# Performance work log

Measured on AMD Instinct MI355X. Metric: run time of the kernel, lower is better.

Reference implementation:

```python
import jax, jax.numpy as jnp
import numpy as np

N = 50000      # nodes
E = 800000     # edges (before self loops)
D_IN = 256
D_H = 256
D_OUT = 64     # num_classes
SLOPE = 0.01   # leaky_relu slope


def setup_inputs() -> dict:
    key = jax.random.key(0)
    ks = jax.random.split(key, 8)
    x = jax.random.normal(ks[0], (N, D_IN), dtype=jnp.float32)
    edge_index = jax.random.randint(ks[1], (2, E), 0, N, dtype=jnp.int32)
    s = 0.05
    W1 = jax.random.normal(ks[2], (D_H, D_IN), dtype=jnp.float32) * s
    b1 = jnp.zeros((D_H,), dtype=jnp.float32)
    W2 = jax.random.normal(ks[3], (D_H, D_H), dtype=jnp.float32) * s
    b2 = jnp.zeros((D_H,), dtype=jnp.float32)
    W3 = jax.random.normal(ks[4], (D_OUT, D_H), dtype=jnp.float32) * s
    b3 = jnp.zeros((D_OUT,), dtype=jnp.float32)
    return {"x": x, "edge_index": edge_index, "W1": W1, "b1": b1,
            "W2": W2, "b2": b2, "W3": W3, "b3": b3}


def _gcn_layer(x, W, b, src, dst):
    # PyG GCNConv: h = x @ W^T; out[dst] += d^{-1/2}[src] d^{-1/2}[dst] * h[src]; out += b
    h = x @ W.T                                             # [N, out]
    ones = jnp.ones(src.shape[0], dtype=h.dtype)
    deg = jax.ops.segment_sum(ones, dst, num_segments=N)    # includes self loops
    dinv = jnp.where(deg > 0, jax.lax.rsqrt(deg), 0.0)
    norm = dinv[src] * dinv[dst]                            # [E+N]
    msg = h[src] * norm[:, None]                            # gather + scale
    out = jax.ops.segment_sum(msg, dst, num_segments=N)     # scatter-add
    return out + b


def reference(x, edge_index, W1, b1, W2, b2, W3, b3):
    src, dst = edge_index[0], edge_index[1]
    loop = jnp.arange(N, dtype=src.dtype)                   # add self loops
    src = jnp.concatenate([src, loop])
    dst = jnp.concatenate([dst, loop])
    act = lambda h: jax.nn.leaky_relu(h, negative_slope=SLOPE)
    h1 = act(_gcn_layer(x, W1, b1, src, dst))
    h2 = act(_gcn_layer(h1, W2, b2, src, dst))
    logits = _gcn_layer(h2, W3, b3, src, dst)               # no activation on last layer
    return (h1, h2, logits)
```

## Files before the change

kernel.cpp:

```cpp
#include <hip/hip_runtime.h>

#define N_NODES 50000
#define E_EDGES 800000
#define SLOPE 0.01f

typedef __attribute__((ext_vector_type(8))) short bf16x8;
typedef __attribute__((ext_vector_type(4))) float floatx4;
typedef __attribute__((ext_vector_type(4))) float f32x4;
typedef __attribute__((ext_vector_type(2))) unsigned int u32x2;

__device__ __forceinline__ unsigned short f2bf(float f) {
    unsigned u = __builtin_bit_cast(unsigned, f);
    unsigned r = (u + 0x7FFFu + ((u >> 16) & 1u)) >> 16;
    return (unsigned short)r;
}
__device__ __forceinline__ float bf2f(unsigned short h) {
    unsigned u = ((unsigned)h) << 16;
    return __builtin_bit_cast(float, u);
}
__device__ __forceinline__ float blo(unsigned u) { return __builtin_bit_cast(float, u << 16); }
__device__ __forceinline__ float bhi(unsigned u) { return __builtin_bit_cast(float, u & 0xFFFF0000u); }

__device__ __forceinline__ void acc8(uint4 v, float a[8]) {
    a[0] += blo(v.x); a[1] += bhi(v.x);
    a[2] += blo(v.y); a[3] += bhi(v.y);
    a[4] += blo(v.z); a[5] += bhi(v.z);
    a[6] += blo(v.w); a[7] += bhi(v.w);
}
__device__ __forceinline__ void acc4(uint2 v, float a[4]) {
    a[0] += blo(v.x); a[1] += bhi(v.x);
    a[2] += blo(v.y); a[3] += bhi(v.y);
}


__device__ __forceinline__ void conv_body(const float* __restrict__ in,
                                          unsigned short* __restrict__ out, int i, int n4) {
    if (i < n4) {
        float4 v = ((const float4*)in)[i];
        ushort4 o;
        o.x = f2bf(v.x); o.y = f2bf(v.y); o.z = f2bf(v.z); o.w = f2bf(v.w);
        ((ushort4*)out)[i] = o;
    }
}

__device__ __forceinline__ void wfrag_body(const float* __restrict__ Wf,
                                           unsigned short* __restrict__ out, int idx, int n4) {
    if (idx >= n4) return;
    int n = idx >> 6;
    int k = (idx & 63) << 2;
    float4 v = ((const float4*)Wf)[idx];
    int jt = n >> 4, lm = n & 15, kk = k >> 5, q = (k >> 3) & 3, e = k & 7;
    int off = ((jt * 8 + kk) * 64 + q * 16 + lm) * 8 + e;
    ushort4 o;
    o.x = f2bf(v.x); o.y = f2bf(v.y); o.z = f2bf(v.z); o.w = f2bf(v.w);
    *(ushort4*)(out + off) = o;
}

#define PREP_HIST_B   3125
#define PREP_CONV_B   12500
#define PREP_W1_B     64
#define PREP_W2_B     64
#define PREP_W3_B     16
#define PREP_TOTAL_B  (PREP_HIST_B + PREP_CONV_B + PREP_W1_B + PREP_W2_B + PREP_W3_B)

__global__ __launch_bounds__(256) void prep0_kernel(
        const float* __restrict__ x, unsigned short* __restrict__ xb,
        const float* __restrict__ W1, unsigned short* __restrict__ W1f,
        const float* __restrict__ W2, unsigned short* __restrict__ W2f,
        const float* __restrict__ W3, unsigned short* __restrict__ W3f,
        const int* __restrict__ dst, int* __restrict__ counts,
        unsigned short* __restrict__ rank) {
    int b = blockIdx.x, tid = threadIdx.x;
    if (b < PREP_HIST_B) {
        int e = b * 256 + tid;
        if (e < E_EDGES) {
            int d = dst[e];
            rank[e] = (unsigned short)atomicAdd(&counts[d], 1);
        }
    } else if (b < PREP_HIST_B + PREP_CONV_B) {
        conv_body(x, xb, (b - PREP_HIST_B) * 256 + tid, N_NODES * 256 / 4);
    } else if (b < PREP_HIST_B + PREP_CONV_B + PREP_W1_B) {
        wfrag_body(W1, W1f, (b - PREP_HIST_B - PREP_CONV_B) * 256 + tid, 16384);
    } else if (b < PREP_HIST_B + PREP_CONV_B + PREP_W1_B + PREP_W2_B) {
        wfrag_body(W2, W2f, (b - PREP_HIST_B - PREP_CONV_B - PREP_W1_B) * 256 + tid, 16384);
    } else {
        wfrag_body(W3, W3f, (b - PREP_HIST_B - PREP_CONV_B - PREP_W1_B - PREP_W2_B) * 256 + tid, 4096);
    }
}


#define SB 1024
__global__ __launch_bounds__(SB) void scan1_dinv_kernel(const int* __restrict__ counts,
                                                        int* __restrict__ partial,
                                                        int* __restrict__ bsum,
                                                        float* __restrict__ dinv) {
    __shared__ int wsum[16];
    int tid = threadIdx.x, lane = tid & 63, wid = tid >> 6;
    int i = blockIdx.x * SB + tid;
    int v = (i < N_NODES) ? counts[i] : 0;
    int x = v;
    #pragma unroll
    for (int off = 1; off < 64; off <<= 1) {
        int y = __shfl_up(x, off, 64);
        if (lane >= off) x += y;
    }
    if (lane == 63) wsum[wid] = x;
    __syncthreads();
    if (wid == 0) {
        int s = (lane < 16) ? wsum[lane] : 0;
        #pragma unroll
        for (int off = 1; off < 16; off <<= 1) {
            int y = __shfl_up(s, off, 64);
            if (lane >= off) s += y;
        }
        if (lane < 16) wsum[lane] = s;
    }
    __syncthreads();
    int woff = wid ? wsum[wid - 1] : 0;
    if (i < N_NODES) {
        partial[i] = woff + x - v;
        dinv[i] = rsqrtf((float)(v + 1));
    }
    if (tid == SB - 1) bsum[blockIdx.x] = woff + x;
}

__global__ __launch_bounds__(256) void scan3b_kernel(int* __restrict__ row_ptr,
                                                     const int* __restrict__ bsum,
                                                     int nb) {
    __shared__ int pref[64];
    int tid = threadIdx.x;
    if (tid < 64) {
        int v = (tid < nb) ? bsum[tid] : 0;
        #pragma unroll
        for (int off = 1; off < 64; off <<= 1) {
            int y = __shfl_up(v, off, 64);
            if (tid >= off) v += y;
        }
        pref[tid] = v;
    }
    __syncthreads();
    int i = blockIdx.x * 256 + tid;
    if (i < N_NODES) {
        int c = i >> 10;
        int off = c ? pref[c - 1] : 0;
        row_ptr[i] += off;
    }
    if (i == 0) row_ptr[N_NODES] = pref[nb - 1];
}


template<int WAVES_M, int WAVES_N, int MT, int NT>
__device__ __forceinline__ void gemm_frag_body(
        int bx, int by, int tid,
        const unsigned short* __restrict__ Ab,
        const unsigned short* __restrict__ Bf,
        const float* __restrict__ dinv,
        unsigned short* __restrict__ C, int M, int Nc) {
    const int wave = tid >> 6, lane = tid & 63;
    const int lm = lane & 15, q = lane >> 4;
    const int bm = bx * (WAVES_M * MT * 16);
    const int bn = by * (WAVES_N * NT * 16);
    const int wm = (wave / WAVES_N) * (MT * 16);
    const int wn = (wave % WAVES_N) * (NT * 16);
    const int jt0 = (bn + wn) >> 4;

    const unsigned short* arow[MT];
    #pragma unroll
    for (int i = 0; i < MT; ++i) {
        int r = bm + wm + i * 16 + lm;
        if (r >= M) r = M - 1;
        arow[i] = Ab + (size_t)r * 256 + q * 8;
    }

    floatx4 acc[MT][NT] = {};

    #pragma unroll
    for (int kk = 0; kk < 8; ++kk) {
        bf16x8 a[MT], b[NT];
        #pragma unroll
        for (int i = 0; i < MT; ++i)
            a[i] = *(const bf16x8*)(arow[i] + kk * 32);
        #pragma unroll
        for (int j = 0; j < NT; ++j)
            b[j] = *(const bf16x8*)(Bf + (((jt0 + j) * 8 + kk) * 64 + lane) * 8);
        #pragma unroll
        for (int i = 0; i < MT; ++i)
            #pragma unroll
            for (int j = 0; j < NT; ++j)
                acc[i][j] = __builtin_amdgcn_mfma_f32_16x16x32_bf16(a[i], b[j], acc[i][j], 0, 0, 0);
    }

    #pragma unroll
    for (int i = 0; i < MT; ++i) {
        int rb = bm + wm + i * 16 + q * 4;
        #pragma unroll
        for (int r = 0; r < 4; ++r) {
            int row = rb + r;
            if (row < M) {
                float dd = dinv[row];
                #pragma unroll
                for (int j = 0; j < NT; ++j)
                    C[(size_t)row * Nc + bn + wn + j * 16 + lm] = f2bf(acc[i][j][r] * dd);
            }
        }
    }
}

__global__ __launch_bounds__(256) void gemm256_kernel(
        const unsigned short* __restrict__ Ab, const unsigned short* __restrict__ Bf,
        const float* __restrict__ dinv, unsigned short* __restrict__ C, int M, int Nc) {
    gemm_frag_body<2, 2, 4, 4>(blockIdx.x, blockIdx.y, threadIdx.x, Ab, Bf, dinv, C, M, Nc);
}

__global__ __launch_bounds__(256) void gemm64_kernel(
        const unsigned short* __restrict__ Ab, const unsigned short* __restrict__ Bf,
        const float* __restrict__ dinv, unsigned short* __restrict__ C, int M, int Nc) {
    gemm_frag_body<4, 1, 4, 4>(blockIdx.x, 0, threadIdx.x, Ab, Bf, dinv, C, M, Nc);
}

#define GEMM1_B 782
__global__ __launch_bounds__(256) void gemm1_place_kernel(
        const unsigned short* __restrict__ Ab, const unsigned short* __restrict__ Bf,
        const float* __restrict__ dinv, unsigned short* __restrict__ C, int M, int Nc,
        const int* __restrict__ src, const int* __restrict__ dst,
        const int* __restrict__ row_ptr, const unsigned short* __restrict__ rank,
        int* __restrict__ col_idx) {
    int b = blockIdx.x;
    if (b < PREP_HIST_B) {
        int e = b * 256 + threadIdx.x;
        if (e < E_EDGES) {
            int d = dst[e];
            int pos = row_ptr[d] + (int)rank[e];
            col_idx[pos] = src[e];
        }
    } else {
        int b2 = b - PREP_HIST_B;
        gemm_frag_body<2, 2, 4, 4>(b2 >> 1, b2 & 1, threadIdx.x, Ab, Bf, dinv, C, M, Nc);
    }
}


template<bool ACT>
__global__ __launch_bounds__(256) void agg256_kernel(
        const int* __restrict__ row_ptr, const int* __restrict__ col_idx,
        const float* __restrict__ dinv, const unsigned short* __restrict__ hs,
        const float* __restrict__ bias,
        float* __restrict__ out, unsigned short* __restrict__ outb) {
    int node = __builtin_amdgcn_readfirstlane(blockIdx.x * 4 + (threadIdx.x >> 6));
    int lane = threadIdx.x & 63;
    int half = lane >> 5, sl = lane & 31;

    float a[8] = {};

    int beg = row_ptr[node], end = row_ptr[node + 1];
    int j = beg;
    for (; j + 8 <= end; j += 8) {
        int s0 = col_idx[j + half];
        int s1 = col_idx[j + 2 + half];
        int s2 = col_idx[j + 4 + half];
        int s3 = col_idx[j + 6 + half];
        uint4 v0 = ((const uint4*)(hs + (size_t)s0 * 256))[sl];
        uint4 v1 = ((const uint4*)(hs + (size_t)s1 * 256))[sl];
        uint4 v2 = ((const uint4*)(hs + (size_t)s2 * 256))[sl];
        uint4 v3 = ((const uint4*)(hs + (size_t)s3 * 256))[sl];
        acc8(v0, a); acc8(v1, a); acc8(v2, a); acc8(v3, a);
    }
    for (; j + 2 <= end; j += 2) {
        int s = col_idx[j + half];
        uint4 v = ((const uint4*)(hs + (size_t)s * 256))[sl];
        acc8(v, a);
    }
    if (j < end && half == 0) {
        int s = col_idx[j];
        uint4 v = ((const uint4*)(hs + (size_t)s * 256))[sl];
        acc8(v, a);
    }

    #pragma unroll
    for (int k = 0; k < 8; ++k) a[k] += __shfl_xor(a[k], 32);

    uint4 sv = ((const uint4*)(hs + (size_t)node * 256))[sl];
    acc8(sv, a);

    int srcl = lane >> 1;
    float t0 = __shfl(a[0], srcl), t1 = __shfl(a[1], srcl);
    float t2 = __shfl(a[2], srcl), t3 = __shfl(a[3], srcl);
    float t4 = __shfl(a[4], srcl), t5 = __shfl(a[5], srcl);
    float t6 = __shfl(a[6], srcl), t7 = __shfl(a[7], srcl);
    bool hi = (lane & 1);
    float f0 = hi ? t4 : t0, f1 = hi ? t5 : t1, f2 = hi ? t6 : t2, f3 = hi ? t7 : t3;

    float dd = dinv[node];
    const float4 b4 = ((const float4*)bias)[lane];
    f0 = fmaf(f0, dd, b4.x); f1 = fmaf(f1, dd, b4.y);
    f2 = fmaf(f2, dd, b4.z); f3 = fmaf(f3, dd, b4.w);
    if (ACT) {
        f0 = f0 > 0.f ? f0 : SLOPE * f0;
        f1 = f1 > 0.f ? f1 : SLOPE * f1;
        f2 = f2 > 0.f ? f2 : SLOPE * f2;
        f3 = f3 > 0.f ? f3 : SLOPE * f3;
    }
    f32x4 o = {f0, f1, f2, f3};
    __builtin_nontemporal_store(o, (f32x4*)(out + (size_t)node * 256) + lane);
    u32x2 obv;
    obv.x = ((unsigned)f2bf(f1) << 16) | f2bf(f0);
    obv.y = ((unsigned)f2bf(f3) << 16) | f2bf(f2);
    __builtin_nontemporal_store(obv, (u32x2*)(outb + (size_t)node * 256) + lane);
}

__global__ __launch_bounds__(256) void agg64_kernel(
        const int* __restrict__ row_ptr, const int* __restrict__ col_idx,
        const float* __restrict__ dinv, const unsigned short* __restrict__ hs,
        const float* __restrict__ bias, float* __restrict__ out) {
    int node = __builtin_amdgcn_readfirstlane(blockIdx.x * 4 + (threadIdx.x >> 6));
    int lane = threadIdx.x & 63;
    int g = lane >> 4, sl = lane & 15;

    float a[4] = {};

    int beg = row_ptr[node], end = row_ptr[node + 1];
    int j = beg;
    for (; j + 8 <= end; j += 8) {
        int s0 = col_idx[j + g];
        int s1 = col_idx[j + 4 + g];
        uint2 v0 = ((const uint2*)(hs + (size_t)s0 * 64))[sl];
        uint2 v1 = ((const uint2*)(hs + (size_t)s1 * 64))[sl];
        acc4(v0, a); acc4(v1, a);
    }
    for (; j + 4 <= end; j += 4) {
        int s = col_idx[j + g];
        uint2 v = ((const uint2*)(hs + (size_t)s * 64))[sl];
        acc4(v, a);
    }
    int rem = end - j;
    if (g < rem) {
        int s = col_idx[j + g];
        uint2 v = ((const uint2*)(hs + (size_t)s * 64))[sl];
        acc4(v, a);
    }

    #pragma unroll
    for (int k = 0; k < 4; ++k) {
        a[k] += __shfl_xor(a[k], 16);
        a[k] += __shfl_xor(a[k], 32);
    }

    uint2 sv = ((const uint2*)(hs + (size_t)node * 64))[sl];
    acc4(sv, a);

    float dd = dinv[node];
    const float4 b4 = ((const float4*)bias)[sl];
    f32x4 o;
    o[0] = fmaf(a[0], dd, b4.x);
    o[1] = fmaf(a[1], dd, b4.y);
    o[2] = fmaf(a[2], dd, b4.z);
    o[3] = fmaf(a[3], dd, b4.w);
    if (g == 0)
        __builtin_nontemporal_store(o, (f32x4*)(out + (size_t)node * 64) + sl);
}


static inline int cdiv(long long a, long long b) { return (int)((a + b - 1) / b); }

extern "C" void kernel_launch(void* const* d_in, const int* in_sizes, int n_in,
                              void* d_out, int out_size, void* d_ws, size_t ws_size,
                              hipStream_t stream) {
    const float* x  = (const float*)d_in[0];
    const int* ei   = (const int*)d_in[1];
    const float* W1 = (const float*)d_in[2];
    const float* b1 = (const float*)d_in[3];
    const float* W2 = (const float*)d_in[4];
    const float* b2 = (const float*)d_in[5];
    const float* W3 = (const float*)d_in[6];
    const float* b3 = (const float*)d_in[7];

    const int* src = ei;
    const int* dst = ei + E_EDGES;

    char* ws = (char*)d_ws;
    int*   counts  = (int*)ws;   ws += 50048 * 4;
    int*   row_ptr = (int*)ws;   ws += 50112 * 4;
    float* dinv    = (float*)ws; ws += 50048 * 4;
    int*   bsum    = (int*)ws;   ws += 64 * 4;
    unsigned short* rank = (unsigned short*)ws; ws += (size_t)E_EDGES * 2;
    int*   col_idx = (int*)ws;   ws += (size_t)E_EDGES * 4;
    unsigned short* W1f = (unsigned short*)ws; ws += 65536 * 2;
    unsigned short* W2f = (unsigned short*)ws; ws += 65536 * 2;
    unsigned short* W3f = (unsigned short*)ws; ws += 16384 * 2;
    unsigned short* hb  = (unsigned short*)ws; ws += (size_t)N_NODES * 256 * 2;
    unsigned short* ob  = (unsigned short*)ws;

    float* out1 = (float*)d_out;
    float* out2 = out1 + (size_t)N_NODES * 256;
    float* out3 = out2 + (size_t)N_NODES * 256;

    const int NB = cdiv(N_NODES, SB);

    (void)hipMemsetAsync(counts, 0, 50048 * sizeof(int), stream);
    prep0_kernel<<<PREP_TOTAL_B, 256, 0, stream>>>(x, ob, W1, W1f, W2, W2f, W3, W3f,
                                                   dst, counts, rank);

    scan1_dinv_kernel<<<NB, SB, 0, stream>>>(counts, row_ptr, bsum, dinv);
    scan3b_kernel<<<cdiv(N_NODES, 256), 256, 0, stream>>>(row_ptr, bsum, NB);

    dim3 g256(cdiv(N_NODES, 128), 2);
    int agg_grid = cdiv(N_NODES, 4);

    gemm1_place_kernel<<<PREP_HIST_B + GEMM1_B, 256, 0, stream>>>(
        ob, W1f, dinv, hb, N_NODES, 256, src, dst, row_ptr, rank, col_idx);
    agg256_kernel<true><<<agg_grid, 256, 0, stream>>>(row_ptr, col_idx, dinv, hb, b1, out1, ob);

    gemm256_kernel<<<g256, 256, 0, stream>>>(ob, W2f, dinv, hb, N_NODES, 256);
    agg256_kernel<true><<<agg_grid, 256, 0, stream>>>(row_ptr, col_idx, dinv, hb, b2, out2, ob);

    gemm64_kernel<<<cdiv(N_NODES, 256), 256, 0, stream>>>(ob, W3f, dinv, hb, N_NODES, 64);
    agg64_kernel<<<agg_grid, 256, 0, stream>>>(row_ptr, col_idx, dinv, hb, b3, out3);
}
```

Baseline: 425.5 us.

## Pad degree counters, pack aggregation accumulators as float2, use cached bf16 stores

The degree-count array is padded to one counter per 128 bytes and placed in the hb buffer, so histogram atomics on different nodes stop sharing cache lines. This costs a memset about 32 times larger. The aggregation kernels now accumulate into float2 vectors so the compiler can emit packed adds. The bf16 copy of each layer's output is written with a normal store instead of a nontemporal one, so the next GEMM can hit it in cache.

```diff
diff --git a/kernel.cpp b/kernel.cpp
--- a/kernel.cpp
+++ b/kernel.cpp
@@ -3,10 +3,12 @@
 #define N_NODES 50000
 #define E_EDGES 800000
 #define SLOPE 0.01f
+#define CSTRIDE 32
 
 typedef __attribute__((ext_vector_type(8))) short bf16x8;
 typedef __attribute__((ext_vector_type(4))) float floatx4;
 typedef __attribute__((ext_vector_type(4))) float f32x4;
+typedef __attribute__((ext_vector_type(2))) float f32x2;
 typedef __attribute__((ext_vector_type(2))) unsigned int u32x2;
 
 __device__ __forceinline__ unsigned short f2bf(float f) {
@@ -20,16 +22,15 @@
 }
 __device__ __forceinline__ float blo(unsigned u) { return __builtin_bit_cast(float, u << 16); }
 __device__ __forceinline__ float bhi(unsigned u) { return __builtin_bit_cast(float, u & 0xFFFF0000u); }
-
-__device__ __forceinline__ void acc8(uint4 v, float a[8]) {
-    a[0] += blo(v.x); a[1] += bhi(v.x);
-    a[2] += blo(v.y); a[3] += bhi(v.y);
-    a[4] += blo(v.z); a[5] += bhi(v.z);
-    a[6] += blo(v.w); a[7] += bhi(v.w);
-}
-__device__ __forceinline__ void acc4(uint2 v, float a[4]) {
-    a[0] += blo(v.x); a[1] += bhi(v.x);
-    a[2] += blo(v.y); a[3] += bhi(v.y);
+__device__ __forceinline__ f32x2 up2(unsigned u) {
+    f32x2 t; t.x = blo(u); t.y = bhi(u); return t;
+}
+
+__device__ __forceinline__ void acc8p(uint4 v, f32x2 a[4]) {
+    a[0] += up2(v.x); a[1] += up2(v.y); a[2] += up2(v.z); a[3] += up2(v.w);
+}
+__device__ __forceinline__ void acc4p(uint2 v, f32x2 a[2]) {
+    a[0] += up2(v.x); a[1] += up2(v.y);
 }
 
 
@@ -75,7 +76,7 @@
         int e = b * 256 + tid;
         if (e < E_EDGES) {
             int d = dst[e];
-            rank[e] = (unsigned short)atomicAdd(&counts[d], 1);
+            rank[e] = (unsigned short)atomicAdd(&counts[(size_t)d * CSTRIDE], 1);
         }
     } else if (b < PREP_HIST_B + PREP_CONV_B) {
         conv_body(x, xb, (b - PREP_HIST_B) * 256 + tid, N_NODES * 256 / 4);
@@ -97,7 +98,7 @@
     __shared__ int wsum[16];
     int tid = threadIdx.x, lane = tid & 63, wid = tid >> 6;
     int i = blockIdx.x * SB + tid;
-    int v = (i < N_NODES) ? counts[i] : 0;
+    int v = (i < N_NODES) ? counts[(size_t)i * CSTRIDE] : 0;
     int x = v;
     #pragma unroll
     for (int off = 1; off < 64; off <<= 1) {
@@ -250,7 +251,7 @@
     int lane = threadIdx.x & 63;
     int half = lane >> 5, sl = lane & 31;
 
-    float a[8] = {};
+    f32x2 a[4] = {};
 
     int beg = row_ptr[node], end = row_ptr[node + 1];
     int j = beg;
@@ -263,30 +264,38 @@
         uint4 v1 = ((const uint4*)(hs + (size_t)s1 * 256))[sl];
         uint4 v2 = ((const uint4*)(hs + (size_t)s2 * 256))[sl];
         uint4 v3 = ((const uint4*)(hs + (size_t)s3 * 256))[sl];
-        acc8(v0, a); acc8(v1, a); acc8(v2, a); acc8(v3, a);
+        acc8p(v0, a); acc8p(v1, a); acc8p(v2, a); acc8p(v3, a);
     }
     for (; j + 2 <= end; j += 2) {
         int s = col_idx[j + half];
         uint4 v = ((const uint4*)(hs + (size_t)s * 256))[sl];
-        acc8(v, a);
+        acc8p(v, a);
     }
     if (j < end && half == 0) {
         int s = col_idx[j];
         uint4 v = ((const uint4*)(hs + (size_t)s * 256))[sl];
-        acc8(v, a);
-    }
-
-    #pragma unroll
-    for (int k = 0; k < 8; ++k) a[k] += __shfl_xor(a[k], 32);
+        acc8p(v, a);
+    }
+
+    float s0 = a[0].x, s1 = a[0].y, s2 = a[1].x, s3 = a[1].y;
+    float s4 = a[2].x, s5 = a[2].y, s6 = a[3].x, s7 = a[3].y;
+
+    s0 += __shfl_xor(s0, 32); s1 += __shfl_xor(s1, 32);
+    s2 += __shfl_xor(s2, 32); s3 += __shfl_xor(s3, 32);
+    s4 += __shfl_xor(s4, 32); s5 += __shfl_xor(s5, 32);
+    s6 += __shfl_xor(s6, 32); s7 += __shfl_xor(s7, 32);
 
     uint4 sv = ((const uint4*)(hs + (size_t)node * 256))[sl];
-    acc8(sv, a);
+    s0 += blo(sv.x); s1 += bhi(sv.x);
+    s2 += blo(sv.y); s3 += bhi(sv.y);
+    s4 += blo(sv.z); s5 += bhi(sv.z);
+    s6 += blo(sv.w); s7 += bhi(sv.w);
 
     int srcl = lane >> 1;
-    float t0 = __shfl(a[0], srcl), t1 = __shfl(a[1], srcl);
-    float t2 = __shfl(a[2], srcl), t3 = __shfl(a[3], srcl);
-    float t4 = __shfl(a[4], srcl), t5 = __shfl(a[5], srcl);
-    float t6 = __shfl(a[6], srcl), t7 = __shfl(a[7], srcl);
+    float t0 = __shfl(s0, srcl), t1 = __shfl(s1, srcl);
+    float t2 = __shfl(s2, srcl), t3 = __shfl(s3, srcl);
+    float t4 = __shfl(s4, srcl), t5 = __shfl(s5, srcl);
+    float t6 = __shfl(s6, srcl), t7 = __shfl(s7, srcl);
     bool hi = (lane & 1);
     float f0 = hi ? t4 : t0, f1 = hi ? t5 : t1, f2 = hi ? t6 : t2, f3 = hi ? t7 : t3;
 
@@ -305,7 +314,7 @@
     u32x2 obv;
     obv.x = ((unsigned)f2bf(f1) << 16) | f2bf(f0);
     obv.y = ((unsigned)f2bf(f3) << 16) | f2bf(f2);
-    __builtin_nontemporal_store(obv, (u32x2*)(outb + (size_t)node * 256) + lane);
+    ((u32x2*)(outb + (size_t)node * 256))[lane] = obv;
 }
 
 __global__ __launch_bounds__(256) void agg64_kernel(
@@ -316,7 +325,7 @@
     int lane = threadIdx.x & 63;
     int g = lane >> 4, sl = lane & 15;
 
-    float a[4] = {};
+    f32x2 a[2] = {};
 
     int beg = row_ptr[node], end = row_ptr[node + 1];
     int j = beg;
@@ -325,36 +334,38 @@
         int s1 = col_idx[j + 4 + g];
         uint2 v0 = ((const uint2*)(hs + (size_t)s0 * 64))[sl];
         uint2 v1 = ((const uint2*)(hs + (size_t)s1 * 64))[sl];
-        acc4(v0, a); acc4(v1, a);
+        acc4p(v0, a); acc4p(v1, a);
     }
     for (; j + 4 <= end; j += 4) {
         int s = col_idx[j + g];
         uint2 v = ((const uint2*)(hs + (size_t)s * 64))[sl];
-        acc4(v, a);
+        acc4p(v, a);
     }
     int rem = end - j;
     if (g < rem) {
         int s = col_idx[j + g];
         uint2 v = ((const uint2*)(hs + (size_t)s * 64))[sl];
-        acc4(v, a);
-    }
-
-    #pragma unroll
-    for (int k = 0; k < 4; ++k) {
-        a[k] += __shfl_xor(a[k], 16);
-        a[k] += __shfl_xor(a[k], 32);
-    }
+        acc4p(v, a);
+    }
+
+    float s0 = a[0].x, s1 = a[0].y, s2 = a[1].x, s3 = a[1].y;
+
+    s0 += __shfl_xor(s0, 16); s0 += __shfl_xor(s0, 32);
+    s1 += __shfl_xor(s1, 16); s1 += __shfl_xor(s1, 32);
+    s2 += __shfl_xor(s2, 16); s2 += __shfl_xor(s2, 32);
+    s3 += __shfl_xor(s3, 16); s3 += __shfl_xor(s3, 32);
 
     uint2 sv = ((const uint2*)(hs + (size_t)node * 64))[sl];
-    acc4(sv, a);
+    s0 += blo(sv.x); s1 += bhi(sv.x);
+    s2 += blo(sv.y); s3 += bhi(sv.y);
 
     float dd = dinv[node];
     const float4 b4 = ((const float4*)bias)[sl];
     f32x4 o;
-    o[0] = fmaf(a[0], dd, b4.x);
-    o[1] = fmaf(a[1], dd, b4.y);
-    o[2] = fmaf(a[2], dd, b4.z);
-    o[3] = fmaf(a[3], dd, b4.w);
+    o[0] = fmaf(s0, dd, b4.x);
+    o[1] = fmaf(s1, dd, b4.y);
+    o[2] = fmaf(s2, dd, b4.z);
+    o[3] = fmaf(s3, dd, b4.w);
     if (g == 0)
         __builtin_nontemporal_store(o, (f32x4*)(out + (size_t)node * 64) + sl);
 }
@@ -378,7 +389,6 @@
     const int* dst = ei + E_EDGES;
 
     char* ws = (char*)d_ws;
-    int*   counts  = (int*)ws;   ws += 50048 * 4;
     int*   row_ptr = (int*)ws;   ws += 50112 * 4;
     float* dinv    = (float*)ws; ws += 50048 * 4;
     int*   bsum    = (int*)ws;   ws += 64 * 4;
@@ -390,13 +400,15 @@
     unsigned short* hb  = (unsigned short*)ws; ws += (size_t)N_NODES * 256 * 2;
     unsigned short* ob  = (unsigned short*)ws;
 
+    int* counts = (int*)hb;
+
     float* out1 = (float*)d_out;
     float* out2 = out1 + (size_t)N_NODES * 256;
     float* out3 = out2 + (size_t)N_NODES * 256;
 
     const int NB = cdiv(N_NODES, SB);
 
-    (void)hipMemsetAsync(counts, 0, 50048 * sizeof(int), stream);
+    (void)hipMemsetAsync(counts, 0, (size_t)50048 * CSTRIDE * sizeof(int), stream);
     prep0_kernel<<<PREP_TOTAL_B, 256, 0, stream>>>(x, ob, W1, W1f, W2, W2f, W3, W3f,
                                                    dst, counts, rank);
 
```

After: 425.4 us. No clear change (-0.0%).
